# Kernel tuning notes

Measured on AMD Instinct MI355X. Metric: run time of the kernel, lower is better.

## Reference

```python
import jax, jax.numpy as jnp
import numpy as np

B, T, V, D = 1024, 20, 10000, 512
H = 64  # actor/critic hidden


def _ln(x, g=None, b=None, eps=1e-5):
    m = x.mean(-1, keepdims=True)
    v = ((x - m) ** 2).mean(-1, keepdims=True)
    y = (x - m) * jax.lax.rsqrt(v + eps)
    return y * g + b if g is not None else y


def setup_inputs() -> dict:
    key = jax.random.key(0)
    ks = jax.random.split(key, 40)
    s = 0.02

    def rn(k, shape, sc=s):
        return jax.random.normal(k, shape, dtype=jnp.float32) * sc

    inp = {
        "image_feature": jax.random.normal(ks[0], (B, 2048), dtype=jnp.float32),
        "box_feature": jax.random.normal(ks[1], (B, 256), dtype=jnp.float32),
        "actions": jax.random.randint(ks[2], (B, T), 0, V),
        # feature_resizer: Linear(2304, D)  (stored [in, out])
        "fr_W": rn(ks[3], (2304, D)), "fr_b": jnp.zeros((D,), jnp.float32),
        # encoder _block dense1 / dense2
        "b1_W1": rn(ks[4], (D, D)), "b1_b1": jnp.zeros((D,), jnp.float32),
        "b1_W2": rn(ks[5], (D, D)), "b1_b2": jnp.zeros((D,), jnp.float32),
        "b2_W1": rn(ks[6], (D, D)), "b2_b1": jnp.zeros((D,), jnp.float32),
        "b2_W2": rn(ks[7], (D, D)), "b2_b2": jnp.zeros((D,), jnp.float32),
        # encoder final LayerNorm (affine) + Linear(D, 512)
        "ln_g": jnp.ones((D,), jnp.float32), "ln_b": jnp.zeros((D,), jnp.float32),
        "enc_W": rn(ks[8], (D, 512)), "enc_b": jnp.zeros((512,), jnp.float32),
        # word embedding
        "emb": rn(ks[9], (V, 512), 1.0),
        # GRUCell(512, 512): gates ordered r,z,n (PyTorch)
        "gru_Wih": rn(ks[10], (512, 3 * 512)), "gru_bih": jnp.zeros((3 * 512,), jnp.float32),
        "gru_Whh": rn(ks[11], (512, 3 * 512)), "gru_bhh": jnp.zeros((3 * 512,), jnp.float32),
        # actor MLP 512->64->64->V
        "act_W1": rn(ks[12], (512, H), 0.05), "act_b1": jnp.zeros((H,), jnp.float32),
        "act_W2": rn(ks[13], (H, H), 0.05), "act_b2": jnp.zeros((H,), jnp.float32),
        "act_W3": rn(ks[14], (H, V), 0.01), "act_b3": jnp.zeros((V,), jnp.float32),
        # critic MLP 512->64->64->1
        "cr_W1": rn(ks[15], (512, H), 0.05), "cr_b1": jnp.zeros((H,), jnp.float32),
        "cr_W2": rn(ks[16], (H, H), 0.05), "cr_b2": jnp.zeros((H,), jnp.float32),
        "cr_W3": rn(ks[17], (H, 1), 0.05), "cr_b3": jnp.zeros((1,), jnp.float32),
        # word_mask buffer: 0 for allowed words, -1000 otherwise
        "word_mask": jnp.where(jnp.arange(V) < V // 2, 0.0, -1000.0).astype(jnp.float32),
    }
    return inp


def reference(image_feature, box_feature, actions,
              fr_W, fr_b,
              b1_W1, b1_b1, b1_W2, b1_b2,
              b2_W1, b2_b1, b2_W2, b2_b2,
              ln_g, ln_b, enc_W, enc_b,
              emb, gru_Wih, gru_bih, gru_Whh, gru_bhh,
              act_W1, act_b1, act_W2, act_b2, act_W3, act_b3,
              cr_W1, cr_b1, cr_W2, cr_b2, cr_W3, cr_b3,
              word_mask):
    gelu = lambda x: jax.nn.gelu(x, approximate=False)

    # get_image_representation: Linear(2304, D) over concat
    x = jnp.concatenate([image_feature, box_feature], axis=1) @ fr_W + fr_b  # [B, D]

    # encoder: _block -> LayerNorm(affine) -> Linear(D, 512)
    y = _ln(x)
    y = gelu(y @ b1_W1 + b1_b1) @ b1_W2 + b1_b2
    y = _ln(y + x)
    blk = x + (gelu(y @ b2_W1 + b2_b1) @ b2_W2 + b2_b2)
    img_rep = _ln(blk, ln_g, ln_b) @ enc_W + enc_b  # [B, 512]

    def step(carry, a_t):
        hx, ix = carry
        # torch code: hx = decoder(hx, ix) -> GRUCell(input=hx, hidden=ix)
        gi = hx @ gru_Wih + gru_bih
        gh = ix @ gru_Whh + gru_bhh
        ir, iz, inn = jnp.split(gi, 3, axis=-1)
        hr, hz, hn = jnp.split(gh, 3, axis=-1)
        r = jax.nn.sigmoid(ir + hr)
        z = jax.nn.sigmoid(iz + hz)
        n = jnp.tanh(inn + r * hn)
        h = (1.0 - z) * n + z * ix  # new hx
        # actor logits + mask + log_softmax
        a = jnp.tanh(h @ act_W1 + act_b1)
        a = jnp.tanh(a @ act_W2 + act_b2)
        logits = a @ act_W3 + act_b3 + word_mask
        logp = jax.nn.log_softmax(logits, axis=-1)  # [B, V]
        lp = jnp.take_along_axis(logp, a_t[:, None], axis=-1)[:, 0]  # [B]
        ent = -jnp.sum(jnp.exp(logp) * logp, axis=-1)  # [B]
        c = jnp.tanh(h @ cr_W1 + cr_b1)
        c = jnp.tanh(c @ cr_W2 + cr_b2)
        val = c @ cr_W3 + cr_b3  # [B, 1]
        ix_new = emb[a_t]  # [B, 512]
        return (h, ix_new), (lp, ent, val)

    init = (img_rep, jnp.zeros_like(img_rep))
    (_, _), (lps, ents, vals) = jax.lax.scan(step, init, actions.T)  # over T
    logprobs = lps.T                     # [B, T]
    entropies = ents.T                   # [B, T]
    values = jnp.transpose(vals, (1, 0, 2))  # [B, T, 1]
    return actions, logprobs, entropies, values
```

## Files before the change

kernel.cpp:

```cpp
#include <hip/hip_runtime.h>
#include <math.h>

#define Tlen 20
#define Vv 10000
#define BT 20480

typedef __attribute__((ext_vector_type(8))) short b16x8;
typedef __attribute__((ext_vector_type(4))) float f32x4;

__device__ __forceinline__ unsigned short f2b(float f){
    union { float f; unsigned u; } v; v.f = f;
    unsigned r = v.u + 0x7FFFu + ((v.u >> 16) & 1u);
    return (unsigned short)(r >> 16);
}
__device__ __forceinline__ float b2f(unsigned short h){
    union { unsigned u; float f; } v; v.u = ((unsigned)h) << 16;
    return v.f;
}
__device__ __forceinline__ void gload16(const void* g, void* l){
    __builtin_amdgcn_global_load_lds(
        (const __attribute__((address_space(1))) unsigned int*)g,
        (__attribute__((address_space(3))) unsigned int*)l, 16, 0, 0);
}
__device__ __forceinline__ float fast_sig(float x){ return 1.f / (1.f + __expf(-x)); }
__device__ __forceinline__ float fast_tanh(float x){ return 1.f - 2.f / (__expf(2.f * x) + 1.f); }

template<int ACT, int OUTF, int OUTB, int AF32, int RES>
__device__ __forceinline__ void gemm_bf_dev(
        const void* __restrict__ Av, const unsigned short* __restrict__ BTp,
        const float* __restrict__ bias, const float* __restrict__ Radd,
        float* __restrict__ Cf, unsigned short* __restrict__ Cb,
        int N, int K, int bx, int by)
{
    __shared__ __align__(16) char As[64 * 80];
    __shared__ __align__(16) char Bs[64 * 80];
    const int tid = threadIdx.x;
    const int wid = tid >> 6, lane = tid & 63;
    const int row0 = by * 64, col0 = bx * 64;
    const int srow = tid >> 2, sslot = tid & 3;
    f32x4 acc[4];
    #pragma unroll
    for (int i = 0; i < 4; i++) acc[i] = (f32x4){0.f, 0.f, 0.f, 0.f};
    const int afoff = (wid * 16 + (lane & 15)) * 80 + (lane >> 4) * 16;
    for (int k0 = 0; k0 < K; k0 += 32) {
        b16x8 av, bv;
        if (AF32) {
            const float* Af = (const float*)Av + (size_t)(row0 + srow) * K + k0 + sslot * 8;
            float4 a0 = *(const float4*)Af;
            float4 a1 = *(const float4*)(Af + 4);
            av[0]=(short)f2b(a0.x); av[1]=(short)f2b(a0.y); av[2]=(short)f2b(a0.z); av[3]=(short)f2b(a0.w);
            av[4]=(short)f2b(a1.x); av[5]=(short)f2b(a1.y); av[6]=(short)f2b(a1.z); av[7]=(short)f2b(a1.w);
        } else {
            av = *(const b16x8*)((const unsigned short*)Av + (size_t)(row0 + srow) * K + k0 + sslot * 8);
        }
        bv = *(const b16x8*)(BTp + (size_t)(col0 + srow) * K + k0 + sslot * 8);
        __syncthreads();
        *(b16x8*)(As + srow * 80 + sslot * 16) = av;
        *(b16x8*)(Bs + srow * 80 + sslot * 16) = bv;
        __syncthreads();
        b16x8 af = *(const b16x8*)(As + afoff);
        #pragma unroll
        for (int ct = 0; ct < 4; ct++) {
            b16x8 bf = *(const b16x8*)(Bs + (ct * 16 + (lane & 15)) * 80 + (lane >> 4) * 16);
            acc[ct] = __builtin_amdgcn_mfma_f32_16x16x32_bf16(af, bf, acc[ct], 0, 0, 0);
        }
    }
    const int orow = row0 + wid * 16 + (lane >> 4) * 4;
    #pragma unroll
    for (int ct = 0; ct < 4; ct++) {
        int col = col0 + ct * 16 + (lane & 15);
        float bb = bias ? bias[col] : 0.f;
        #pragma unroll
        for (int r = 0; r < 4; r++) {
            float v = acc[ct][r] + bb;
            if (ACT == 1) v = 0.5f * v * (1.f + erff(v * 0.70710678118654752f));
            else if (ACT == 2) v = tanhf(v);
            size_t idx = (size_t)(orow + r) * N + col;
            if (RES) v += Radd[idx];
            if (OUTF) Cf[idx] = v;
            if (OUTB) Cb[idx] = f2b(v);
        }
    }
}

template<int ACT, int OUTF, int OUTB, int AF32, int RES>
__global__ __launch_bounds__(256) void gemm_bf_k(
        const void* __restrict__ Av, const unsigned short* __restrict__ BTp,
        const float* __restrict__ bias, const float* __restrict__ Radd,
        float* __restrict__ Cf, unsigned short* __restrict__ Cb, int N, int K)
{
    gemm_bf_dev<ACT, OUTF, OUTB, AF32, RES>(Av, BTp, bias, Radd, Cf, Cb, N, K,
            blockIdx.x, blockIdx.y);
}

template<int ACT, int AFFINE, int OUTF, int OUTB>
__global__ __launch_bounds__(256) void gemm_ln_bf_k(
        const float* __restrict__ A, const unsigned short* __restrict__ BTp,
        const float* __restrict__ bias, const float* __restrict__ g,
        const float* __restrict__ be, float* __restrict__ Cf,
        unsigned short* __restrict__ Cb)
{
    __shared__ __align__(16) char As[64 * 80];
    __shared__ __align__(16) char Bs[64 * 80];
    __shared__ float sMean[64], sInv[64];
    const int tid = threadIdx.x;
    const int wid = tid >> 6, lane = tid & 63;
    const int row0 = blockIdx.y * 64, col0 = blockIdx.x * 64;
    const int srow = tid >> 2, sslot = tid & 3;
    {
        const float4* Ar = (const float4*)(A + (size_t)(row0 + srow) * 512 + sslot * 128);
        float s = 0.f, s2 = 0.f;
        #pragma unroll
        for (int i = 0; i < 32; i++) {
            float4 v = Ar[i];
            s += v.x + v.y + v.z + v.w;
            s2 += v.x * v.x + v.y * v.y + v.z * v.z + v.w * v.w;
        }
        s += __shfl_xor(s, 1, 64);  s += __shfl_xor(s, 2, 64);
        s2 += __shfl_xor(s2, 1, 64); s2 += __shfl_xor(s2, 2, 64);
        if (sslot == 0) {
            float m = s * (1.f / 512.f);
            sMean[srow] = m;
            sInv[srow] = rsqrtf(s2 * (1.f / 512.f) - m * m + 1e-5f);
        }
    }
    __syncthreads();
    f32x4 acc[4];
    #pragma unroll
    for (int i = 0; i < 4; i++) acc[i] = (f32x4){0.f, 0.f, 0.f, 0.f};
    const int afoff = (wid * 16 + (lane & 15)) * 80 + (lane >> 4) * 16;
    for (int k0 = 0; k0 < 512; k0 += 32) {
        const float* Af = A + (size_t)(row0 + srow) * 512 + k0 + sslot * 8;
        float4 a0 = *(const float4*)Af;
        float4 a1 = *(const float4*)(Af + 4);
        const float m = sMean[srow], iv = sInv[srow];
        float y[8] = {(a0.x-m)*iv, (a0.y-m)*iv, (a0.z-m)*iv, (a0.w-m)*iv,
                      (a1.x-m)*iv, (a1.y-m)*iv, (a1.z-m)*iv, (a1.w-m)*iv};
        if (AFFINE) {
            const int kb = k0 + sslot * 8;
            float4 g0 = *(const float4*)(g + kb), g1 = *(const float4*)(g + kb + 4);
            float4 e0 = *(const float4*)(be + kb), e1 = *(const float4*)(be + kb + 4);
            y[0] = y[0]*g0.x + e0.x; y[1] = y[1]*g0.y + e0.y;
            y[2] = y[2]*g0.z + e0.z; y[3] = y[3]*g0.w + e0.w;
            y[4] = y[4]*g1.x + e1.x; y[5] = y[5]*g1.y + e1.y;
            y[6] = y[6]*g1.z + e1.z; y[7] = y[7]*g1.w + e1.w;
        }
        b16x8 av;
        #pragma unroll
        for (int i = 0; i < 8; i++) av[i] = (short)f2b(y[i]);
        b16x8 bv = *(const b16x8*)(BTp + (size_t)(col0 + srow) * 512 + k0 + sslot * 8);
        __syncthreads();
        *(b16x8*)(As + srow * 80 + sslot * 16) = av;
        *(b16x8*)(Bs + srow * 80 + sslot * 16) = bv;
        __syncthreads();
        b16x8 af = *(const b16x8*)(As + afoff);
        #pragma unroll
        for (int ct = 0; ct < 4; ct++) {
            b16x8 bf = *(const b16x8*)(Bs + (ct * 16 + (lane & 15)) * 80 + (lane >> 4) * 16);
            acc[ct] = __builtin_amdgcn_mfma_f32_16x16x32_bf16(af, bf, acc[ct], 0, 0, 0);
        }
    }
    const int orow = row0 + wid * 16 + (lane >> 4) * 4;
    #pragma unroll
    for (int ct = 0; ct < 4; ct++) {
        int col = col0 + ct * 16 + (lane & 15);
        float bb = bias[col];
        #pragma unroll
        for (int r = 0; r < 4; r++) {
            float v = acc[ct][r] + bb;
            if (ACT == 1) v = 0.5f * v * (1.f + erff(v * 0.70710678118654752f));
            size_t idx = (size_t)(orow + r) * 512 + col;
            if (OUTF) Cf[idx] = v;
            if (OUTB) Cb[idx] = f2b(v);
        }
    }
}

__device__ __forceinline__ void gemm_big_dev(
        const unsigned short* __restrict__ Aptr, const unsigned short* __restrict__ Bptr,
        unsigned short* __restrict__ C, int N, int K, int idx, int nwgx, int nwg)
{
    __shared__ __align__(16) unsigned short As[2][128 * 32];
    __shared__ __align__(16) unsigned short Bs[2][128 * 32];
    const int tid = threadIdx.x, w = tid >> 6, lane = tid & 63;
    const int l15 = lane & 15, lh = lane >> 4;
    const int q = nwg >> 3, r = nwg & 7;
    const int xcd = idx & 7, pos = idx >> 3;
    const int wgid = (xcd < r ? xcd * (q + 1) : r * (q + 1) + (xcd - r) * q) + pos;
    const int bx = wgid % nwgx, by = wgid / nwgx;
    const int row0 = by * 128, col0 = bx * 128;
    const int wr = w >> 1, wc = w & 1;
    const int slw = ((lane & 3) ^ ((lane >> 2) & 3) ^ ((lane >> 4) & 3)) & 3;
    const int pa  = (lh ^ (l15 & 3) ^ ((l15 >> 2) & 3)) & 3;
    f32x4 acc[4][4];
    #pragma unroll
    for (int i = 0; i < 4; i++)
        #pragma unroll
        for (int j = 0; j < 4; j++) acc[i][j] = (f32x4){0.f, 0.f, 0.f, 0.f};
    const int nkt = K >> 5;
    #pragma unroll
    for (int c = 0; c < 2; c++) {
        int ch = w * 2 + c, rr = ch * 16 + (lane >> 2);
        gload16(Aptr + (size_t)(row0 + rr) * K + slw * 8, &As[0][ch * 512]);
        gload16(Bptr + (size_t)(col0 + rr) * K + slw * 8, &Bs[0][ch * 512]);
    }
    __syncthreads();
    for (int kt = 0; kt < nkt; kt++) {
        const int buf = kt & 1;
        if (kt + 1 < nkt) {
            const int k0 = (kt + 1) << 5;
            #pragma unroll
            for (int c = 0; c < 2; c++) {
                int ch = w * 2 + c, rr = ch * 16 + (lane >> 2);
                gload16(Aptr + (size_t)(row0 + rr) * K + k0 + slw * 8, &As[buf ^ 1][ch * 512]);
                gload16(Bptr + (size_t)(col0 + rr) * K + k0 + slw * 8, &Bs[buf ^ 1][ch * 512]);
            }
        }
        b16x8 af[4], bf[4];
        #pragma unroll
        for (int f = 0; f < 4; f++) {
            af[f] = *(const b16x8*)(&As[buf][(wr * 64 + f * 16 + l15) * 32 + pa * 8]);
            bf[f] = *(const b16x8*)(&Bs[buf][(wc * 64 + f * 16 + l15) * 32 + pa * 8]);
        }
        #pragma unroll
        for (int i = 0; i < 4; i++)
            #pragma unroll
            for (int j = 0; j < 4; j++)
                acc[i][j] = __builtin_amdgcn_mfma_f32_16x16x32_bf16(af[i], bf[j], acc[i][j], 0, 0, 0);
        __syncthreads();
    }
    #pragma unroll
    for (int i = 0; i < 4; i++) {
        const int orow = row0 + wr * 64 + i * 16 + lh * 4;
        #pragma unroll
        for (int j = 0; j < 4; j++) {
            const int col = col0 + wc * 64 + j * 16 + l15;
            #pragma unroll
            for (int rr2 = 0; rr2 < 4; rr2++)
                C[(size_t)(orow + rr2) * N + col] = f2b(acc[i][j][rr2]);
        }
    }
}

__global__ __launch_bounds__(256) void big_fr_k(
        const unsigned short* __restrict__ embB, const unsigned short* __restrict__ WhhT,
        unsigned short* __restrict__ GHemb,
        const unsigned short* __restrict__ A0, const unsigned short* __restrict__ frWT,
        const float* __restrict__ fr_b, float* __restrict__ Xe)
{
    const int bid = blockIdx.x;
    if (bid < 128) {
        gemm_bf_dev<0, 1, 0, 0, 0>(A0, frWT, fr_b, nullptr, Xe, nullptr,
                512, 2304, bid & 7, bid >> 3);
    } else {
        gemm_big_dev(embB, WhhT, GHemb, 1536, 512, bid - 128, 12, 948);
    }
}

__device__ void tileT_dev(const float* __restrict__ W, unsigned short* __restrict__ WT,
        int K, int N, int bx, int by)
{
    __shared__ float s[32][33];
    const int n0 = bx * 32, k0 = by * 32;
    const int tx = threadIdx.x & 31, ty = threadIdx.x >> 5;
    #pragma unroll
    for (int i = 0; i < 32; i += 8) {
        int k = k0 + ty + i, n = n0 + tx;
        s[ty + i][tx] = (k < K && n < N) ? W[(size_t)k * N + n] : 0.f;
    }
    __syncthreads();
    #pragma unroll
    for (int i = 0; i < 32; i += 8) {
        int n = n0 + ty + i, k = k0 + tx;
        if (n < N && k < K) WT[(size_t)n * K + k] = f2b(s[tx][ty + i]);
    }
}

__global__ __launch_bounds__(256) void prep_all_k(
        const float* __restrict__ Wih, const float* __restrict__ Whh,
        const float* __restrict__ frW, const float* __restrict__ b1W1,
        const float* __restrict__ b1W2, const float* __restrict__ b2W1,
        const float* __restrict__ b2W2, const float* __restrict__ encW,
        const float* __restrict__ aW1, const float* __restrict__ cW1,
        const float* __restrict__ aW3, const float* __restrict__ aW2,
        const float* __restrict__ cW2, const float* __restrict__ ab1,
        const float* __restrict__ cb1, const float* __restrict__ ab2,
        const float* __restrict__ cb2, const float* __restrict__ emb,
        const float* __restrict__ img, const float* __restrict__ box,
        unsigned short* __restrict__ WihT, unsigned short* __restrict__ WhhT,
        unsigned short* __restrict__ frWT, unsigned short* __restrict__ b1W1T,
        unsigned short* __restrict__ b1W2T, unsigned short* __restrict__ b2W1T,
        unsigned short* __restrict__ b2W2T, unsigned short* __restrict__ encWT,
        unsigned short* __restrict__ W1cT, unsigned short* __restrict__ W2cT,
        unsigned short* __restrict__ WT3, float* __restrict__ b1c,
        float* __restrict__ b2c, unsigned short* __restrict__ embB,
        unsigned short* __restrict__ A0)
{
    int bid = blockIdx.x;
    const int tid = threadIdx.x;
    if (bid < 768) { tileT_dev(Wih, WihT, 512, 1536, bid % 48, bid / 48); return; }
    bid -= 768;
    if (bid < 768) { tileT_dev(Whh, WhhT, 512, 1536, bid % 48, bid / 48); return; }
    bid -= 768;
    if (bid < 1152) { tileT_dev(frW, frWT, 2304, 512, bid % 16, bid / 16); return; }
    bid -= 1152;
    if (bid < 256) { tileT_dev(b1W1, b1W1T, 512, 512, bid % 16, bid / 16); return; }
    bid -= 256;
    if (bid < 256) { tileT_dev(b1W2, b1W2T, 512, 512, bid % 16, bid / 16); return; }
    bid -= 256;
    if (bid < 256) { tileT_dev(b2W1, b2W1T, 512, 512, bid % 16, bid / 16); return; }
    bid -= 256;
    if (bid < 256) { tileT_dev(b2W2, b2W2T, 512, 512, bid % 16, bid / 16); return; }
    bid -= 256;
    if (bid < 256) { tileT_dev(encW, encWT, 512, 512, bid % 16, bid / 16); return; }
    bid -= 256;
    if (bid < 32) { tileT_dev(aW1, W1cT, 512, 64, bid % 2, bid / 2); return; }
    bid -= 32;
    if (bid < 32) { tileT_dev(cW1, W1cT + (size_t)64 * 512, 512, 64, bid % 2, bid / 2); return; }
    bid -= 32;
    if (bid < 626) { tileT_dev(aW3, WT3, 64, 10000, bid % 313, bid / 313); return; }
    bid -= 626;
    if (bid < 64) {
        int idx = bid * 256 + tid;
        int j = idx >> 7, k = idx & 127;
        float v = 0.f;
        if (j < 64 && k < 64) v = aW2[(size_t)k * 64 + j];
        else if (j >= 64 && k >= 64) v = cW2[(size_t)(k - 64) * 64 + (j - 64)];
        W2cT[idx] = f2b(v);
        return;
    }
    bid -= 64;
    if (bid < 1) {
        if (tid < 128) b1c[tid] = (tid < 64) ? ab1[tid] : cb1[tid - 64];
        else { int i = tid - 128; b2c[i] = (i < 64) ? ab2[i] : cb2[i - 64]; }
        return;
    }
    bid -= 1;
    if (bid < 5056) {
        int idx = bid * 256 + tid;
        int row = idx >> 7, c4 = (idx & 127) * 4;
        float4 v = {0.f, 0.f, 0.f, 0.f};
        if (row < Vv) v = *(const float4*)(emb + (size_t)row * 512 + c4);
        ushort4 o; o.x = f2b(v.x); o.y = f2b(v.y); o.z = f2b(v.z); o.w = f2b(v.w);
        *(ushort4*)(embB + (size_t)row * 512 + c4) = o;
        return;
    }
    bid -= 5056;
    {
        int idx = bid * 256 + tid;
        int row = idx / 576, c4 = (idx - row * 576) * 4;
        float4 v = (c4 < 2048) ? *(const float4*)(img + (size_t)row * 2048 + c4)
                               : *(const float4*)(box + (size_t)row * 256 + (c4 - 2048));
        ushort4 o; o.x = f2b(v.x); o.y = f2b(v.y); o.z = f2b(v.z); o.w = f2b(v.w);
        *(ushort4*)(A0 + (size_t)row * 2304 + c4) = o;
    }
}

__global__ __launch_bounds__(256) void gru_step3_k(
        const unsigned short* __restrict__ Hprev,
        const unsigned short* __restrict__ WihT,
        const float* __restrict__ bih, const float* __restrict__ bhh,
        const unsigned short* __restrict__ GHemb,
        const float* __restrict__ emb, const int* __restrict__ acts, int t,
        unsigned short* __restrict__ Hout)
{
    __shared__ __align__(16) unsigned short sB[48 * 512];
    const int tid = threadIdx.x, w = tid >> 6, lane = tid & 63;
    const int l15 = lane & 15, lh = lane >> 4;
    const int d0 = blockIdx.x * 16;
    const int rows0 = blockIdx.y * 64 + w * 16;
    const unsigned short* Arow = Hprev + (size_t)(rows0 + l15) * 512 + lh * 8;
    b16x8 a[16];
    #pragma unroll
    for (int kk = 0; kk < 16; kk++) a[kk] = *(const b16x8*)(Arow + kk * 32);
    #pragma unroll
    for (int c = 0; c < 12; c++) {
        const int ch = w * 12 + c;
        const int g = ch >> 4, col = ch & 15;
        const int sl = lane ^ (ch & 7);
        gload16(WihT + (size_t)(g * 512 + d0 + col) * 512 + sl * 8, &sB[ch * 512]);
    }
    __syncthreads();
    f32x4 ar = (f32x4){0.f,0.f,0.f,0.f}, az = ar, an = ar;
    #pragma unroll
    for (int kk = 0; kk < 16; kk++) {
        const int sl = ((kk * 4 + lh) ^ (l15 & 7));
        b16x8 b0 = *(const b16x8*)(&sB[(l15) * 512 + sl * 8]);
        b16x8 b1 = *(const b16x8*)(&sB[(16 + l15) * 512 + sl * 8]);
        b16x8 b2 = *(const b16x8*)(&sB[(32 + l15) * 512 + sl * 8]);
        ar = __builtin_amdgcn_mfma_f32_16x16x32_bf16(a[kk], b0, ar, 0, 0, 0);
        az = __builtin_amdgcn_mfma_f32_16x16x32_bf16(a[kk], b1, az, 0, 0, 0);
        an = __builtin_amdgcn_mfma_f32_16x16x32_bf16(a[kk], b2, an, 0, 0, 0);
    }
    const int d = d0 + l15;
    const float bi0 = bih[d], bi1 = bih[512 + d], bi2 = bih[1024 + d];
    const float bh0 = bhh[d], bh1 = bhh[512 + d], bh2 = bhh[1024 + d];
    #pragma unroll
    for (int reg = 0; reg < 4; reg++) {
        const int row = rows0 + lh * 4 + reg;
        float hr = bh0, hz = bh1, hn = bh2, ix = 0.f;
        if (t) {
            const int ap = acts[row * Tlen + t - 1];
            const size_t gb = (size_t)ap * 1536;
            hr += b2f(GHemb[gb + d]);
            hz += b2f(GHemb[gb + 512 + d]);
            hn += b2f(GHemb[gb + 1024 + d]);
            ix = emb[(size_t)ap * 512 + d];
        }
        const float rr = fast_sig(ar[reg] + bi0 + hr);
        const float zz = fast_sig(az[reg] + bi1 + hz);
        const float nn = fast_tanh(an[reg] + bi2 + rr * hn);
        Hout[(size_t)row * 512 + d] = f2b((1.f - zz) * nn + zz * ix);
    }
}

__global__ __launch_bounds__(256) void logits3_k(const unsigned short* __restrict__ A2b,
        const unsigned short* __restrict__ WT3, const float* __restrict__ b3,
        const float* __restrict__ wmask, float* __restrict__ Spart,
        float* __restrict__ Wmpart)
{
    __shared__ __align__(16) char Bs[64 * 144];
    __shared__ float bmS[64];
    const int tid = threadIdx.x, wid = tid >> 6, lane = tid & 63;
    const int r0 = blockIdx.x * 64;
    const int c0 = blockIdx.y * 640;
    const int cend = (c0 + 640 < 5056) ? c0 + 640 : 5056;
    const size_t abase = (size_t)(r0 + wid * 16 + (lane & 15)) * 128 + (lane >> 4) * 8;
    const b16x8 af0 = *(const b16x8*)(A2b + abase);
    const b16x8 af1 = *(const b16x8*)(A2b + abase + 32);
    float S[4] = {0.f, 0.f, 0.f, 0.f}, Wm[4] = {0.f, 0.f, 0.f, 0.f};
    for (int cc = c0; cc < cend; cc += 64) {
        __syncthreads();
        #pragma unroll
        for (int i = 0; i < 2; i++) {
            int e = tid + i * 256;
            int rr = e >> 3, slot = e & 7;
            b16x8 wv = *(const b16x8*)(WT3 + (size_t)(cc + rr) * 64 + slot * 8);
            *(b16x8*)(Bs + rr * 144 + slot * 16) = wv;
        }
        if (tid < 64) bmS[tid] = b3[cc + tid] + wmask[cc + tid];
        __syncthreads();
        #pragma unroll
        for (int ct = 0; ct < 4; ct++) {
            const int colb = (ct * 16 + (lane & 15)) * 144 + (lane >> 4) * 16;
            b16x8 bf0 = *(const b16x8*)(Bs + colb);
            b16x8 bf1 = *(const b16x8*)(Bs + colb + 64);
            f32x4 acc = (f32x4){0.f, 0.f, 0.f, 0.f};
            acc = __builtin_amdgcn_mfma_f32_16x16x32_bf16(af0, bf0, acc, 0, 0, 0);
            acc = __builtin_amdgcn_mfma_f32_16x16x32_bf16(af1, bf1, acc, 0, 0, 0);
            const float bm = bmS[ct * 16 + (lane & 15)];
            #pragma unroll
            for (int r = 0; r < 4; r++) {
                float l = acc[r] + bm;
                float e = __expf(l);
                S[r] += e;
                Wm[r] = fmaf(e, l, Wm[r]);
            }
        }
    }
    #pragma unroll
    for (int r = 0; r < 4; r++) {
        float s = S[r], w = Wm[r];
        #pragma unroll
        for (int o = 1; o < 16; o <<= 1) {
            s += __shfl_xor(s, o, 64);
            w += __shfl_xor(w, o, 64);
        }
        if ((lane & 15) == 0) {
            int row = r0 + wid * 16 + (lane >> 4) * 4 + r;
            Spart[blockIdx.y * BT + row] = s;
            Wmpart[blockIdx.y * BT + row] = w;
        }
    }
}

__global__ __launch_bounds__(256) void tail_k(const float* __restrict__ Spart,
        const float* __restrict__ Wmpart, const unsigned short* __restrict__ L2b,
        const unsigned short* __restrict__ WT3, const float* __restrict__ b3,
        const float* __restrict__ wmask, const int* __restrict__ acts,
        const float* __restrict__ cw3, const float* __restrict__ cb3,
        float* __restrict__ out)
{
    const int bid = blockIdx.x, tid = threadIdx.x;
    if (bid < 80) {
        const int rt = bid * 256 + tid;
        float s = 0.f, wm = 0.f;
        #pragma unroll
        for (int j = 0; j < 8; j++) { s += Spart[j * BT + rt]; wm += Wmpart[j * BT + rt]; }
        const float l = logf(s);
        const int t = rt >> 10, b = rt & 1023;
        out[2 * BT + b * Tlen + t] = l - wm / s;
    } else if (bid < 160) {
        const int rt = (bid - 80) * 256 + tid;
        float s = 0.f;
        #pragma unroll
        for (int j = 0; j < 8; j++) s += Spart[j * BT + rt];
        const int t = rt >> 10, b = rt & 1023;
        const int a = acts[b * Tlen + t];
        const unsigned short* ar = L2b + (size_t)rt * 128;
        const unsigned short* wr = WT3 + (size_t)a * 64;
        float dot = 0.f;
        #pragma unroll 16
        for (int k = 0; k < 64; k++) dot = fmaf(b2f(ar[k]), b2f(wr[k]), dot);
        out[BT + b * Tlen + t] = dot + b3[a] + wmask[a] - logf(s);
    } else if (bid < 240) {
        const int rt = (bid - 160) * 256 + tid;
        const unsigned short* c = L2b + (size_t)rt * 128 + 64;
        float s = cb3[0];
        #pragma unroll 16
        for (int k = 0; k < 64; k++) s = fmaf(b2f(c[k]), cw3[k], s);
        const int t = rt >> 10, b = rt & 1023;
        out[3 * BT + b * Tlen + t] = s;
    } else {
        const int rt = (bid - 240) * 256 + tid;
        out[rt] = (float)acts[rt];
    }
}

extern "C" void kernel_launch(void* const* d_in, const int* in_sizes, int n_in,
                              void* d_out, int out_size, void* d_ws, size_t ws_size,
                              hipStream_t stream)
{
    const float* img  = (const float*)d_in[0];
    const float* box  = (const float*)d_in[1];
    const int*   acts = (const int*)d_in[2];
    const float* fr_W = (const float*)d_in[3];
    const float* fr_b = (const float*)d_in[4];
    const float* b1W1 = (const float*)d_in[5];
    const float* b1b1 = (const float*)d_in[6];
    const float* b1W2 = (const float*)d_in[7];
    const float* b1b2 = (const float*)d_in[8];
    const float* b2W1 = (const float*)d_in[9];
    const float* b2b1 = (const float*)d_in[10];
    const float* b2W2 = (const float*)d_in[11];
    const float* b2b2 = (const float*)d_in[12];
    const float* lng  = (const float*)d_in[13];
    const float* lnb  = (const float*)d_in[14];
    const float* encW = (const float*)d_in[15];
    const float* encb = (const float*)d_in[16];
    const float* emb  = (const float*)d_in[17];
    const float* Wih  = (const float*)d_in[18];
    const float* bih  = (const float*)d_in[19];
    const float* Whh  = (const float*)d_in[20];
    const float* bhh  = (const float*)d_in[21];
    const float* aW1  = (const float*)d_in[22];
    const float* ab1  = (const float*)d_in[23];
    const float* aW2  = (const float*)d_in[24];
    const float* ab2  = (const float*)d_in[25];
    const float* aW3  = (const float*)d_in[26];
    const float* ab3  = (const float*)d_in[27];
    const float* cW1  = (const float*)d_in[28];
    const float* cb1  = (const float*)d_in[29];
    const float* cW2  = (const float*)d_in[30];
    const float* cb2  = (const float*)d_in[31];
    const float* cW3  = (const float*)d_in[32];
    const float* cb3  = (const float*)d_in[33];
    const float* wmask= (const float*)d_in[34];
    float* out = (float*)d_out;

    char* w = (char*)d_ws;
    unsigned short* WihT  = (unsigned short*)w; w += (size_t)786432 * 2;
    unsigned short* WhhT  = (unsigned short*)w; w += (size_t)786432 * 2;
    unsigned short* frWT  = (unsigned short*)w; w += (size_t)1179648 * 2;
    unsigned short* b1W1T = (unsigned short*)w; w += (size_t)262144 * 2;
    unsigned short* b1W2T = (unsigned short*)w; w += (size_t)262144 * 2;
    unsigned short* b2W1T = (unsigned short*)w; w += (size_t)262144 * 2;
    unsigned short* b2W2T = (unsigned short*)w; w += (size_t)262144 * 2;
    unsigned short* encWT = (unsigned short*)w; w += (size_t)262144 * 2;
    unsigned short* W1cT  = (unsigned short*)w; w += (size_t)65536 * 2;
    unsigned short* W2cT  = (unsigned short*)w; w += (size_t)16384 * 2;
    unsigned short* WT3   = (unsigned short*)w; w += (size_t)640000 * 2;
    float* b1c = (float*)w;                     w += 128 * 4;
    float* b2c = (float*)w;                     w += 128 * 4;
    unsigned short* embB  = (unsigned short*)w; w += (size_t)10112 * 512 * 2;
    unsigned short* GHemb = (unsigned short*)w; w += (size_t)10112 * 1536 * 2;
    unsigned short* HALLb = (unsigned short*)w; w += (size_t)10485760 * 2;
    unsigned short* L1b   = (unsigned short*)w; w += (size_t)2621440 * 2;
    unsigned short* L2b   = (unsigned short*)w; w += (size_t)2621440 * 2;
    unsigned short* HB0   = (unsigned short*)w; w += (size_t)524288 * 2;
    float* Spart = (float*)w;                   w += (size_t)8 * BT * 4;
    float* Wmpart= (float*)w;                   w += (size_t)8 * BT * 4;
    unsigned short* A0 = (unsigned short*)w;    w += (size_t)2359296 * 2;
    float* Xe  = (float*)w;                     w += (size_t)524288 * 4;
    float* T2  = (float*)w;                     w += (size_t)524288 * 4;
    float* Sf  = (float*)w;                     w += (size_t)524288 * 4;
    unsigned short* T1b = (unsigned short*)w;   w += (size_t)524288 * 2;
    unsigned short* T3b = (unsigned short*)w;   w += (size_t)524288 * 2;

    const dim3 blk(256);

    prep_all_k<<<12083, blk, 0, stream>>>(Wih, Whh, fr_W, b1W1, b1W2, b2W1, b2W2,
            encW, aW1, cW1, aW3, aW2, cW2, ab1, cb1, ab2, cb2, emb, img, box,
            WihT, WhhT, frWT, b1W1T, b1W2T, b2W1T, b2W2T, encWT, W1cT, W2cT,
            WT3, b1c, b2c, embB, A0);

    big_fr_k<<<1076, blk, 0, stream>>>(embB, WhhT, GHemb, A0, frWT, fr_b, Xe);

    gemm_ln_bf_k<1, 0, 0, 1><<<dim3(8, 16), blk, 0, stream>>>(Xe, b1W1T, b1b1,
            nullptr, nullptr, nullptr, T1b);
    gemm_bf_k<0, 1, 0, 0, 1><<<dim3(8, 16), blk, 0, stream>>>(T1b, b1W2T, b1b2,
            Xe, T2, nullptr, 512, 512);
    gemm_ln_bf_k<1, 0, 0, 1><<<dim3(8, 16), blk, 0, stream>>>(T2, b2W1T, b2b1,
            nullptr, nullptr, nullptr, T3b);
    gemm_bf_k<0, 1, 0, 0, 1><<<dim3(8, 16), blk, 0, stream>>>(T3b, b2W2T, b2b2,
            Xe, Sf, nullptr, 512, 512);
    gemm_ln_bf_k<0, 1, 0, 1><<<dim3(8, 16), blk, 0, stream>>>(Sf, encWT, encb,
            lng, lnb, nullptr, HB0);

    for (int t = 0; t < Tlen; ++t) {
        const unsigned short* Hprev = t ? HALLb + (size_t)(t - 1) * 524288 : HB0;
        gru_step3_k<<<dim3(32, 16), blk, 0, stream>>>(Hprev, WihT, bih, bhh,
                GHemb, emb, acts, t, HALLb + (size_t)t * 524288);
    }

    gemm_bf_k<2, 0, 1, 0, 0><<<dim3(2, 320), blk, 0, stream>>>(HALLb, W1cT, b1c,
            nullptr, nullptr, L1b, 128, 512);
    gemm_bf_k<2, 0, 1, 0, 0><<<dim3(2, 320), blk, 0, stream>>>(L1b, W2cT, b2c,
            nullptr, nullptr, L2b, 128, 128);
    logits3_k<<<dim3(320, 8), blk, 0, stream>>>(L2b, WT3, ab3, wmask, Spart, Wmpart);
    tail_k<<<320, blk, 0, stream>>>(Spart, Wmpart, L2b, WT3, ab3, wmask, acts,
            cW3, cb3, out);
}
```

Baseline: 380.4 us.

## Software-pipeline actor MLP and logits into the GRU scan launches

The 20 serial GRU step launches each used only 512 blocks. The actor MLP layers and the logits reduction now ride in the same launches, lagged by one, two and three steps, so their work overlaps the scan across 23 launches. Weight-prep kernels are also regrouped: Wih and the small transposes move into the big GEMM launch, and only the inputs of the big GEMM stay in the first prep kernel. This adds three extra launches, a larger shared-memory footprint per block (48KB) that may lower occupancy for the GRU body, and splits logits into 16 partials.

```diff
diff --git a/kernel.cpp b/kernel.cpp
--- a/kernel.cpp
+++ b/kernel.cpp
@@ -4,6 +4,7 @@
 #define Tlen 20
 #define Vv 10000
 #define BT 20480
+#define NPART 16
 
 typedef __attribute__((ext_vector_type(8))) short b16x8;
 typedef __attribute__((ext_vector_type(4))) float f32x4;
@@ -26,14 +27,14 @@
 __device__ __forceinline__ float fast_tanh(float x){ return 1.f - 2.f / (__expf(2.f * x) + 1.f); }
 
 template<int ACT, int OUTF, int OUTB, int AF32, int RES>
-__device__ __forceinline__ void gemm_bf_dev(
+__device__ __forceinline__ void gemm_bf_body(char* smem,
         const void* __restrict__ Av, const unsigned short* __restrict__ BTp,
         const float* __restrict__ bias, const float* __restrict__ Radd,
         float* __restrict__ Cf, unsigned short* __restrict__ Cb,
         int N, int K, int bx, int by)
 {
-    __shared__ __align__(16) char As[64 * 80];
-    __shared__ __align__(16) char Bs[64 * 80];
+    char* As = smem;
+    char* Bs = smem + 64 * 80;
     const int tid = threadIdx.x;
     const int wid = tid >> 6, lane = tid & 63;
     const int row0 = by * 64, col0 = bx * 64;
@@ -89,8 +90,9 @@
         const float* __restrict__ bias, const float* __restrict__ Radd,
         float* __restrict__ Cf, unsigned short* __restrict__ Cb, int N, int K)
 {
-    gemm_bf_dev<ACT, OUTF, OUTB, AF32, RES>(Av, BTp, bias, Radd, Cf, Cb, N, K,
-            blockIdx.x, blockIdx.y);
+    __shared__ __align__(16) char smem[10240];
+    gemm_bf_body<ACT, OUTF, OUTB, AF32, RES>(smem, Av, BTp, bias, Radd, Cf, Cb,
+            N, K, blockIdx.x, blockIdx.y);
 }
 
 template<int ACT, int AFFINE, int OUTF, int OUTB>
@@ -176,12 +178,12 @@
     }
 }
 
-__device__ __forceinline__ void gemm_big_dev(
+__device__ __forceinline__ void gemm_big_body(char* smem,
         const unsigned short* __restrict__ Aptr, const unsigned short* __restrict__ Bptr,
         unsigned short* __restrict__ C, int N, int K, int idx, int nwgx, int nwg)
 {
-    __shared__ __align__(16) unsigned short As[2][128 * 32];
-    __shared__ __align__(16) unsigned short Bs[2][128 * 32];
+    unsigned short* As0 = (unsigned short*)smem;
+    unsigned short* Bs0 = As0 + 2 * 128 * 32;
     const int tid = threadIdx.x, w = tid >> 6, lane = tid & 63;
     const int l15 = lane & 15, lh = lane >> 4;
     const int q = nwg >> 3, r = nwg & 7;
@@ -201,8 +203,8 @@
     #pragma unroll
     for (int c = 0; c < 2; c++) {
         int ch = w * 2 + c, rr = ch * 16 + (lane >> 2);
-        gload16(Aptr + (size_t)(row0 + rr) * K + slw * 8, &As[0][ch * 512]);
-        gload16(Bptr + (size_t)(col0 + rr) * K + slw * 8, &Bs[0][ch * 512]);
+        gload16(Aptr + (size_t)(row0 + rr) * K + slw * 8, As0 + ch * 512);
+        gload16(Bptr + (size_t)(col0 + rr) * K + slw * 8, Bs0 + ch * 512);
     }
     __syncthreads();
     for (int kt = 0; kt < nkt; kt++) {
@@ -212,15 +214,15 @@
             #pragma unroll
             for (int c = 0; c < 2; c++) {
                 int ch = w * 2 + c, rr = ch * 16 + (lane >> 2);
-                gload16(Aptr + (size_t)(row0 + rr) * K + k0 + slw * 8, &As[buf ^ 1][ch * 512]);
-                gload16(Bptr + (size_t)(col0 + rr) * K + k0 + slw * 8, &Bs[buf ^ 1][ch * 512]);
+                gload16(Aptr + (size_t)(row0 + rr) * K + k0 + slw * 8, As0 + (buf ^ 1) * 4096 + ch * 512);
+                gload16(Bptr + (size_t)(col0 + rr) * K + k0 + slw * 8, Bs0 + (buf ^ 1) * 4096 + ch * 512);
             }
         }
         b16x8 af[4], bf[4];
         #pragma unroll
         for (int f = 0; f < 4; f++) {
-            af[f] = *(const b16x8*)(&As[buf][(wr * 64 + f * 16 + l15) * 32 + pa * 8]);
-            bf[f] = *(const b16x8*)(&Bs[buf][(wc * 64 + f * 16 + l15) * 32 + pa * 8]);
+            af[f] = *(const b16x8*)(As0 + buf * 4096 + (wr * 64 + f * 16 + l15) * 32 + pa * 8);
+            bf[f] = *(const b16x8*)(Bs0 + buf * 4096 + (wc * 64 + f * 16 + l15) * 32 + pa * 8);
         }
         #pragma unroll
         for (int i = 0; i < 4; i++)
@@ -242,83 +244,107 @@
     }
 }
 
+__device__ void tileT_body(char* smem, const float* __restrict__ W,
+        unsigned short* __restrict__ WT, int K, int N, int bx, int by)
+{
+    float* s = (float*)smem;
+    const int n0 = bx * 32, k0 = by * 32;
+    const int tx = threadIdx.x & 31, ty = threadIdx.x >> 5;
+    #pragma unroll
+    for (int i = 0; i < 32; i += 8) {
+        int k = k0 + ty + i, n = n0 + tx;
+        s[(ty + i) * 33 + tx] = (k < K && n < N) ? W[(size_t)k * N + n] : 0.f;
+    }
+    __syncthreads();
+    #pragma unroll
+    for (int i = 0; i < 32; i += 8) {
+        int n = n0 + ty + i, k = k0 + tx;
+        if (n < N && k < K) WT[(size_t)n * K + k] = f2b(s[tx * 33 + ty + i]);
+    }
+}
+
+__global__ __launch_bounds__(256) void prep1_k(
+        const float* __restrict__ Whh, const float* __restrict__ frW,
+        const float* __restrict__ emb, const float* __restrict__ img,
+        const float* __restrict__ box,
+        unsigned short* __restrict__ WhhT, unsigned short* __restrict__ frWT,
+        unsigned short* __restrict__ embB, unsigned short* __restrict__ A0)
+{
+    __shared__ __align__(16) char smem[4224];
+    int bid = blockIdx.x;
+    const int tid = threadIdx.x;
+    if (bid < 768) { tileT_body(smem, Whh, WhhT, 512, 1536, bid % 48, bid / 48); return; }
+    bid -= 768;
+    if (bid < 1152) { tileT_body(smem, frW, frWT, 2304, 512, bid % 16, bid / 16); return; }
+    bid -= 1152;
+    if (bid < 5056) {
+        int idx = bid * 256 + tid;
+        int row = idx >> 7, c4 = (idx & 127) * 4;
+        float4 v = {0.f, 0.f, 0.f, 0.f};
+        if (row < Vv) v = *(const float4*)(emb + (size_t)row * 512 + c4);
+        ushort4 o; o.x = f2b(v.x); o.y = f2b(v.y); o.z = f2b(v.z); o.w = f2b(v.w);
+        *(ushort4*)(embB + (size_t)row * 512 + c4) = o;
+        return;
+    }
+    bid -= 5056;
+    {
+        int idx = bid * 256 + tid;
+        int row = idx / 576, c4 = (idx - row * 576) * 4;
+        float4 v = (c4 < 2048) ? *(const float4*)(img + (size_t)row * 2048 + c4)
+                               : *(const float4*)(box + (size_t)row * 256 + (c4 - 2048));
+        ushort4 o; o.x = f2b(v.x); o.y = f2b(v.y); o.z = f2b(v.z); o.w = f2b(v.w);
+        *(ushort4*)(A0 + (size_t)row * 2304 + c4) = o;
+    }
+}
+
 __global__ __launch_bounds__(256) void big_fr_k(
         const unsigned short* __restrict__ embB, const unsigned short* __restrict__ WhhT,
         unsigned short* __restrict__ GHemb,
         const unsigned short* __restrict__ A0, const unsigned short* __restrict__ frWT,
-        const float* __restrict__ fr_b, float* __restrict__ Xe)
-{
-    const int bid = blockIdx.x;
-    if (bid < 128) {
-        gemm_bf_dev<0, 1, 0, 0, 0>(A0, frWT, fr_b, nullptr, Xe, nullptr,
-                512, 2304, bid & 7, bid >> 3);
-    } else {
-        gemm_big_dev(embB, WhhT, GHemb, 1536, 512, bid - 128, 12, 948);
-    }
-}
-
-__device__ void tileT_dev(const float* __restrict__ W, unsigned short* __restrict__ WT,
-        int K, int N, int bx, int by)
-{
-    __shared__ float s[32][33];
-    const int n0 = bx * 32, k0 = by * 32;
-    const int tx = threadIdx.x & 31, ty = threadIdx.x >> 5;
-    #pragma unroll
-    for (int i = 0; i < 32; i += 8) {
-        int k = k0 + ty + i, n = n0 + tx;
-        s[ty + i][tx] = (k < K && n < N) ? W[(size_t)k * N + n] : 0.f;
-    }
-    __syncthreads();
-    #pragma unroll
-    for (int i = 0; i < 32; i += 8) {
-        int n = n0 + ty + i, k = k0 + tx;
-        if (n < N && k < K) WT[(size_t)n * K + k] = f2b(s[tx][ty + i]);
-    }
-}
-
-__global__ __launch_bounds__(256) void prep_all_k(
-        const float* __restrict__ Wih, const float* __restrict__ Whh,
-        const float* __restrict__ frW, const float* __restrict__ b1W1,
+        const float* __restrict__ fr_b, float* __restrict__ Xe,
+        const float* __restrict__ Wih, const float* __restrict__ b1W1,
         const float* __restrict__ b1W2, const float* __restrict__ b2W1,
         const float* __restrict__ b2W2, const float* __restrict__ encW,
         const float* __restrict__ aW1, const float* __restrict__ cW1,
         const float* __restrict__ aW3, const float* __restrict__ aW2,
         const float* __restrict__ cW2, const float* __restrict__ ab1,
         const float* __restrict__ cb1, const float* __restrict__ ab2,
-        const float* __restrict__ cb2, const float* __restrict__ emb,
-        const float* __restrict__ img, const float* __restrict__ box,
-        unsigned short* __restrict__ WihT, unsigned short* __restrict__ WhhT,
-        unsigned short* __restrict__ frWT, unsigned short* __restrict__ b1W1T,
+        const float* __restrict__ cb2,
+        unsigned short* __restrict__ WihT, unsigned short* __restrict__ b1W1T,
         unsigned short* __restrict__ b1W2T, unsigned short* __restrict__ b2W1T,
         unsigned short* __restrict__ b2W2T, unsigned short* __restrict__ encWT,
         unsigned short* __restrict__ W1cT, unsigned short* __restrict__ W2cT,
         unsigned short* __restrict__ WT3, float* __restrict__ b1c,
-        float* __restrict__ b2c, unsigned short* __restrict__ embB,
-        unsigned short* __restrict__ A0)
-{
+        float* __restrict__ b2c)
+{
+    __shared__ __align__(16) char smem[32768];
     int bid = blockIdx.x;
     const int tid = threadIdx.x;
-    if (bid < 768) { tileT_dev(Wih, WihT, 512, 1536, bid % 48, bid / 48); return; }
+    if (bid < 128) {
+        gemm_bf_body<0, 1, 0, 0, 0>(smem, A0, frWT, fr_b, nullptr, Xe, nullptr,
+                512, 2304, bid & 7, bid >> 3);
+        return;
+    }
+    bid -= 128;
+    if (bid < 948) { gemm_big_body(smem, embB, WhhT, GHemb, 1536, 512, bid, 12, 948); return; }
+    bid -= 948;
+    if (bid < 768) { tileT_body(smem, Wih, WihT, 512, 1536, bid % 48, bid / 48); return; }
     bid -= 768;
-    if (bid < 768) { tileT_dev(Whh, WhhT, 512, 1536, bid % 48, bid / 48); return; }
-    bid -= 768;
-    if (bid < 1152) { tileT_dev(frW, frWT, 2304, 512, bid % 16, bid / 16); return; }
-    bid -= 1152;
-    if (bid < 256) { tileT_dev(b1W1, b1W1T, 512, 512, bid % 16, bid / 16); return; }
+    if (bid < 256) { tileT_body(smem, b1W1, b1W1T, 512, 512, bid % 16, bid / 16); return; }
     bid -= 256;
-    if (bid < 256) { tileT_dev(b1W2, b1W2T, 512, 512, bid % 16, bid / 16); return; }
+    if (bid < 256) { tileT_body(smem, b1W2, b1W2T, 512, 512, bid % 16, bid / 16); return; }
     bid -= 256;
-    if (bid < 256) { tileT_dev(b2W1, b2W1T, 512, 512, bid % 16, bid / 16); return; }
+    if (bid < 256) { tileT_body(smem, b2W1, b2W1T, 512, 512, bid % 16, bid / 16); return; }
     bid -= 256;
-    if (bid < 256) { tileT_dev(b2W2, b2W2T, 512, 512, bid % 16, bid / 16); return; }
+    if (bid < 256) { tileT_body(smem, b2W2, b2W2T, 512, 512, bid % 16, bid / 16); return; }
     bid -= 256;
-    if (bid < 256) { tileT_dev(encW, encWT, 512, 512, bid % 16, bid / 16); return; }
+    if (bid < 256) { tileT_body(smem, encW, encWT, 512, 512, bid % 16, bid / 16); return; }
     bid -= 256;
-    if (bid < 32) { tileT_dev(aW1, W1cT, 512, 64, bid % 2, bid / 2); return; }
+    if (bid < 32) { tileT_body(smem, aW1, W1cT, 512, 64, bid % 2, bid / 2); return; }
     bid -= 32;
-    if (bid < 32) { tileT_dev(cW1, W1cT + (size_t)64 * 512, 512, 64, bid % 2, bid / 2); return; }
+    if (bid < 32) { tileT_body(smem, cW1, W1cT + (size_t)64 * 512, 512, 64, bid % 2, bid / 2); return; }
     bid -= 32;
-    if (bid < 626) { tileT_dev(aW3, WT3, 64, 10000, bid % 313, bid / 313); return; }
+    if (bid < 626) { tileT_body(smem, aW3, WT3, 64, 10000, bid % 313, bid / 313); return; }
     bid -= 626;
     if (bid < 64) {
         int idx = bid * 256 + tid;
@@ -330,45 +356,25 @@
         return;
     }
     bid -= 64;
-    if (bid < 1) {
+    {
         if (tid < 128) b1c[tid] = (tid < 64) ? ab1[tid] : cb1[tid - 64];
         else { int i = tid - 128; b2c[i] = (i < 64) ? ab2[i] : cb2[i - 64]; }
-        return;
-    }
-    bid -= 1;
-    if (bid < 5056) {
-        int idx = bid * 256 + tid;
-        int row = idx >> 7, c4 = (idx & 127) * 4;
-        float4 v = {0.f, 0.f, 0.f, 0.f};
-        if (row < Vv) v = *(const float4*)(emb + (size_t)row * 512 + c4);
-        ushort4 o; o.x = f2b(v.x); o.y = f2b(v.y); o.z = f2b(v.z); o.w = f2b(v.w);
-        *(ushort4*)(embB + (size_t)row * 512 + c4) = o;
-        return;
-    }
-    bid -= 5056;
-    {
-        int idx = bid * 256 + tid;
-        int row = idx / 576, c4 = (idx - row * 576) * 4;
-        float4 v = (c4 < 2048) ? *(const float4*)(img + (size_t)row * 2048 + c4)
-                               : *(const float4*)(box + (size_t)row * 256 + (c4 - 2048));
-        ushort4 o; o.x = f2b(v.x); o.y = f2b(v.y); o.z = f2b(v.z); o.w = f2b(v.w);
-        *(ushort4*)(A0 + (size_t)row * 2304 + c4) = o;
-    }
-}
-
-__global__ __launch_bounds__(256) void gru_step3_k(
+    }
+}
+
+__device__ __forceinline__ void gru_step_body(char* smem,
         const unsigned short* __restrict__ Hprev,
         const unsigned short* __restrict__ WihT,
         const float* __restrict__ bih, const float* __restrict__ bhh,
         const unsigned short* __restrict__ GHemb,
         const float* __restrict__ emb, const int* __restrict__ acts, int t,
-        unsigned short* __restrict__ Hout)
-{
-    __shared__ __align__(16) unsigned short sB[48 * 512];
+        unsigned short* __restrict__ Hout, int bx, int by)
+{
+    unsigned short* sB = (unsigned short*)smem;
     const int tid = threadIdx.x, w = tid >> 6, lane = tid & 63;
     const int l15 = lane & 15, lh = lane >> 4;
-    const int d0 = blockIdx.x * 16;
-    const int rows0 = blockIdx.y * 64 + w * 16;
+    const int d0 = bx * 16;
+    const int rows0 = by * 64 + w * 16;
     const unsigned short* Arow = Hprev + (size_t)(rows0 + l15) * 512 + lh * 8;
     b16x8 a[16];
     #pragma unroll
@@ -378,16 +384,16 @@
         const int ch = w * 12 + c;
         const int g = ch >> 4, col = ch & 15;
         const int sl = lane ^ (ch & 7);
-        gload16(WihT + (size_t)(g * 512 + d0 + col) * 512 + sl * 8, &sB[ch * 512]);
+        gload16(WihT + (size_t)(g * 512 + d0 + col) * 512 + sl * 8, sB + ch * 512);
     }
     __syncthreads();
     f32x4 ar = (f32x4){0.f,0.f,0.f,0.f}, az = ar, an = ar;
     #pragma unroll
     for (int kk = 0; kk < 16; kk++) {
         const int sl = ((kk * 4 + lh) ^ (l15 & 7));
-        b16x8 b0 = *(const b16x8*)(&sB[(l15) * 512 + sl * 8]);
-        b16x8 b1 = *(const b16x8*)(&sB[(16 + l15) * 512 + sl * 8]);
-        b16x8 b2 = *(const b16x8*)(&sB[(32 + l15) * 512 + sl * 8]);
+        b16x8 b0 = *(const b16x8*)(sB + (l15) * 512 + sl * 8);
+        b16x8 b1 = *(const b16x8*)(sB + (16 + l15) * 512 + sl * 8);
+        b16x8 b2 = *(const b16x8*)(sB + (32 + l15) * 512 + sl * 8);
         ar = __builtin_amdgcn_mfma_f32_16x16x32_bf16(a[kk], b0, ar, 0, 0, 0);
         az = __builtin_amdgcn_mfma_f32_16x16x32_bf16(a[kk], b1, az, 0, 0, 0);
         an = __builtin_amdgcn_mfma_f32_16x16x32_bf16(a[kk], b2, an, 0, 0, 0);
@@ -414,17 +420,16 @@
     }
 }
 
-__global__ __launch_bounds__(256) void logits3_k(const unsigned short* __restrict__ A2b,
-        const unsigned short* __restrict__ WT3, const float* __restrict__ b3,
-        const float* __restrict__ wmask, float* __restrict__ Spart,
-        float* __restrict__ Wmpart)
-{
-    __shared__ __align__(16) char Bs[64 * 144];
-    __shared__ float bmS[64];
+__device__ __forceinline__ void logits_body(char* smem,
+        const unsigned short* __restrict__ A2b, const unsigned short* __restrict__ WT3,
+        const float* __restrict__ b3, const float* __restrict__ wmask,
+        float* __restrict__ Spart, float* __restrict__ Wmpart, int r0, int by)
+{
+    char* Bs = smem;
+    float* bmS = (float*)(smem + 9216);
     const int tid = threadIdx.x, wid = tid >> 6, lane = tid & 63;
-    const int r0 = blockIdx.x * 64;
-    const int c0 = blockIdx.y * 640;
-    const int cend = (c0 + 640 < 5056) ? c0 + 640 : 5056;
+    const int c0 = by * 320;
+    int cend = c0 + 320; if (cend > 5056) cend = 5056;
     const size_t abase = (size_t)(r0 + wid * 16 + (lane & 15)) * 128 + (lane >> 4) * 8;
     const b16x8 af0 = *(const b16x8*)(A2b + abase);
     const b16x8 af1 = *(const b16x8*)(A2b + abase + 32);
@@ -468,9 +473,59 @@
         }
         if ((lane & 15) == 0) {
             int row = r0 + wid * 16 + (lane >> 4) * 4 + r;
-            Spart[blockIdx.y * BT + row] = s;
-            Wmpart[blockIdx.y * BT + row] = w;
-        }
+            Spart[by * BT + row] = s;
+            Wmpart[by * BT + row] = w;
+        }
+    }
+}
+
+__global__ __launch_bounds__(256) void scanfuse_k(int t,
+        const unsigned short* __restrict__ HB0, unsigned short* __restrict__ HALLb,
+        const unsigned short* __restrict__ WihT,
+        const float* __restrict__ bih, const float* __restrict__ bhh,
+        const unsigned short* __restrict__ GHemb, const float* __restrict__ emb,
+        const int* __restrict__ acts,
+        const unsigned short* __restrict__ W1cT, const float* __restrict__ b1c,
+        const unsigned short* __restrict__ W2cT, const float* __restrict__ b2c,
+        unsigned short* __restrict__ L1b, unsigned short* __restrict__ L2b,
+        const unsigned short* __restrict__ WT3, const float* __restrict__ b3,
+        const float* __restrict__ wmask, float* __restrict__ Spart,
+        float* __restrict__ Wmpart)
+{
+    __shared__ __align__(16) char smem[49152];
+    int bid = blockIdx.x;
+    if (bid < 512) {
+        if (t < Tlen) {
+            const unsigned short* Hprev = t ? HALLb + (size_t)(t - 1) * 524288 : HB0;
+            gru_step_body(smem, Hprev, WihT, bih, bhh, GHemb, emb, acts, t,
+                    HALLb + (size_t)t * 524288, bid & 31, bid >> 5);
+        }
+        return;
+    }
+    bid -= 512;
+    if (bid < 32) {
+        const int t1 = t - 1;
+        if (t1 >= 0 && t1 < Tlen)
+            gemm_bf_body<2, 0, 1, 0, 0>(smem, HALLb + (size_t)t1 * 524288, W1cT, b1c,
+                    nullptr, nullptr, L1b + (size_t)t1 * 131072, 128, 512,
+                    bid & 1, bid >> 1);
+        return;
+    }
+    bid -= 32;
+    if (bid < 32) {
+        const int t2 = t - 2;
+        if (t2 >= 0 && t2 < Tlen)
+            gemm_bf_body<2, 0, 1, 0, 0>(smem, L1b + (size_t)t2 * 131072, W2cT, b2c,
+                    nullptr, nullptr, L2b + (size_t)t2 * 131072, 128, 128,
+                    bid & 1, bid >> 1);
+        return;
+    }
+    bid -= 32;
+    {
+        const int t3 = t - 3;
+        if (t3 >= 0 && t3 < Tlen)
+            logits_body(smem, L2b, WT3, b3, wmask, Spart, Wmpart,
+                    t3 * 1024 + (bid & 15) * 64, bid >> 4);
     }
 }
 
@@ -486,7 +541,7 @@
         const int rt = bid * 256 + tid;
         float s = 0.f, wm = 0.f;
         #pragma unroll
-        for (int j = 0; j < 8; j++) { s += Spart[j * BT + rt]; wm += Wmpart[j * BT + rt]; }
+        for (int j = 0; j < NPART; j++) { s += Spart[j * BT + rt]; wm += Wmpart[j * BT + rt]; }
         const float l = logf(s);
         const int t = rt >> 10, b = rt & 1023;
         out[2 * BT + b * Tlen + t] = l - wm / s;
@@ -494,7 +549,7 @@
         const int rt = (bid - 80) * 256 + tid;
         float s = 0.f;
         #pragma unroll
-        for (int j = 0; j < 8; j++) s += Spart[j * BT + rt];
+        for (int j = 0; j < NPART; j++) s += Spart[j * BT + rt];
         const int t = rt >> 10, b = rt & 1023;
         const int a = acts[b * Tlen + t];
         const unsigned short* ar = L2b + (size_t)rt * 128;
@@ -578,8 +633,8 @@
     unsigned short* L1b   = (unsigned short*)w; w += (size_t)2621440 * 2;
     unsigned short* L2b   = (unsigned short*)w; w += (size_t)2621440 * 2;
     unsigned short* HB0   = (unsigned short*)w; w += (size_t)524288 * 2;
-    float* Spart = (float*)w;                   w += (size_t)8 * BT * 4;
-    float* Wmpart= (float*)w;                   w += (size_t)8 * BT * 4;
+    float* Spart = (float*)w;                   w += (size_t)NPART * BT * 4;
+    float* Wmpart= (float*)w;                   w += (size_t)NPART * BT * 4;
     unsigned short* A0 = (unsigned short*)w;    w += (size_t)2359296 * 2;
     float* Xe  = (float*)w;                     w += (size_t)524288 * 4;
     float* T2  = (float*)w;                     w += (size_t)524288 * 4;
@@ -589,12 +644,12 @@
 
     const dim3 blk(256);
 
-    prep_all_k<<<12083, blk, 0, stream>>>(Wih, Whh, fr_W, b1W1, b1W2, b2W1, b2W2,
-            encW, aW1, cW1, aW3, aW2, cW2, ab1, cb1, ab2, cb2, emb, img, box,
-            WihT, WhhT, frWT, b1W1T, b1W2T, b2W1T, b2W2T, encWT, W1cT, W2cT,
-            WT3, b1c, b2c, embB, A0);
-
-    big_fr_k<<<1076, blk, 0, stream>>>(embB, WhhT, GHemb, A0, frWT, fr_b, Xe);
+    prep1_k<<<9280, blk, 0, stream>>>(Whh, fr_W, emb, img, box, WhhT, frWT, embB, A0);
+
+    big_fr_k<<<3879, blk, 0, stream>>>(embB, WhhT, GHemb, A0, frWT, fr_b, Xe,
+            Wih, b1W1, b1W2, b2W1, b2W2, encW, aW1, cW1, aW3, aW2, cW2,
+            ab1, cb1, ab2, cb2,
+            WihT, b1W1T, b1W2T, b2W1T, b2W2T, encWT, W1cT, W2cT, WT3, b1c, b2c);
 
     gemm_ln_bf_k<1, 0, 0, 1><<<dim3(8, 16), blk, 0, stream>>>(Xe, b1W1T, b1b1,
             nullptr, nullptr, nullptr, T1b);
@@ -607,17 +662,12 @@
     gemm_ln_bf_k<0, 1, 0, 1><<<dim3(8, 16), blk, 0, stream>>>(Sf, encWT, encb,
             lng, lnb, nullptr, HB0);
 
-    for (int t = 0; t < Tlen; ++t) {
-        const unsigned short* Hprev = t ? HALLb + (size_t)(t - 1) * 524288 : HB0;
-        gru_step3_k<<<dim3(32, 16), blk, 0, stream>>>(Hprev, WihT, bih, bhh,
-                GHemb, emb, acts, t, HALLb + (size_t)t * 524288);
-    }
-
-    gemm_bf_k<2, 0, 1, 0, 0><<<dim3(2, 320), blk, 0, stream>>>(HALLb, W1cT, b1c,
-            nullptr, nullptr, L1b, 128, 512);
-    gemm_bf_k<2, 0, 1, 0, 0><<<dim3(2, 320), blk, 0, stream>>>(L1b, W2cT, b2c,
-            nullptr, nullptr, L2b, 128, 128);
-    logits3_k<<<dim3(320, 8), blk, 0, stream>>>(L2b, WT3, ab3, wmask, Spart, Wmpart);
+    for (int t = 0; t < Tlen + 3; ++t) {
+        scanfuse_k<<<832, blk, 0, stream>>>(t, HB0, HALLb, WihT, bih, bhh,
+                GHemb, emb, acts, W1cT, b1c, W2cT, b2c, L1b, L2b,
+                WT3, ab3, wmask, Spart, Wmpart);
+    }
+
     tail_k<<<320, blk, 0, stream>>>(Spart, Wmpart, L2b, WT3, ab3, wmask, acts,
             cW3, cb3, out);
 }
```

Measured after the change: 450.8 us. +18.5%, slower.
